# Optimization experiments

Measured on AMD Instinct MI355X. Metric: run time of the kernel, lower is better.

## Reference

```python
import jax, jax.numpy as jnp
import numpy as np

N_HEADS = 16
N_KV_HEADS = 4
WINDOW = 128
THETA = 10000.0


def _rope_cos_sin(T, half):
    inv = 1.0 / (THETA ** (jnp.arange(half, dtype=jnp.float32) / half))
    f = jnp.arange(T, dtype=jnp.float32)[:, None] * inv[None, :]  # (T, half)
    return jnp.cos(f), jnp.sin(f)


def _apply_rope(x, cos, sin):
    # x: (B, H, T, hd); interleaved (real, imag) pairs like torch view_as_complex
    xr, xi = x[..., 0::2], x[..., 1::2]
    out_r = xr * cos - xi * sin
    out_i = xr * sin + xi * cos
    return jnp.stack([out_r, out_i], axis=-1).reshape(x.shape)


def setup_inputs() -> dict:
    key = jax.random.key(0)
    ks = jax.random.split(key, 6)
    B, T, C = 1, 4096, 2048
    kvC = (C // N_HEADS) * N_KV_HEADS
    return {
        "x": jax.random.normal(ks[0], (B, T, C), dtype=jnp.float32),
        "wq": jax.random.normal(ks[1], (C, C), dtype=jnp.float32) * 0.02,
        "wk": jax.random.normal(ks[2], (C, kvC), dtype=jnp.float32) * 0.02,
        "wv": jax.random.normal(ks[3], (C, kvC), dtype=jnp.float32) * 0.02,
        "wo": jax.random.normal(ks[4], (C, C), dtype=jnp.float32) * 0.02,
        "sink": jnp.zeros((1, N_HEADS, 1, 1), dtype=jnp.float32),
    }


def reference(x, wq, wk, wv, wo, sink):
    B, T, C = x.shape
    hd = C // N_HEADS
    n_rep = N_HEADS // N_KV_HEADS

    q = (x @ wq).reshape(B, T, N_HEADS, hd).transpose(0, 2, 1, 3)    # (B,H,T,hd)
    k = (x @ wk).reshape(B, T, N_KV_HEADS, hd).transpose(0, 2, 1, 3)  # (B,Hkv,T,hd)
    v = (x @ wv).reshape(B, T, N_KV_HEADS, hd).transpose(0, 2, 1, 3)

    cos, sin = _rope_cos_sin(T, hd // 2)  # (T, hd/2), broadcasts over (B,H,T,hd/2)
    q = _apply_rope(q, cos, sin)
    k = _apply_rope(k, cos, sin)

    # GQA head expansion (repeat_interleave over head dim)
    k = jnp.repeat(k, n_rep, axis=1)
    v = jnp.repeat(v, n_rep, axis=1)

    att = jnp.einsum("bhqd,bhkd->bhqk", q, k) * (hd ** -0.5) + sink

    # symmetric sliding-window band: |i - j| <= window//2
    idx = jnp.arange(T)
    band = jnp.abs(idx[:, None] - idx[None, :]) <= (WINDOW // 2)
    att = jnp.where(band[None, None, :, :], att, -jnp.inf)

    att = jax.nn.softmax(att, axis=-1)
    # torch code replaces NaN rows (fully-masked) with uniform; band always has diag so no-op
    att = jnp.where(jnp.isnan(att), 1.0 / T, att)

    out = jnp.einsum("bhqk,bhkd->bqhd", att, v).reshape(B, T, C)
    return out @ wo
```

## Files before the change

kernel.cpp:

```cpp
#include <hip/hip_runtime.h>
#include <stdint.h>

#define T_SEQ 4096
#define C_DIM 2048
#define HD 128

typedef unsigned short ushort_t;
typedef __attribute__((ext_vector_type(8))) short shortx8;
typedef __attribute__((ext_vector_type(4))) float floatx4;
typedef __attribute__((ext_vector_type(8))) unsigned short u16x8;
typedef __attribute__((ext_vector_type(4))) unsigned short u16x4;

__device__ __forceinline__ ushort_t f2bf(float f) {
  union { float f; uint32_t u; } v; v.f = f;
  v.u += 0x7fffu + ((v.u >> 16) & 1u);
  return (ushort_t)(v.u >> 16);
}
__device__ __forceinline__ void load_lds16(const ushort_t* g, ushort_t* l) {
  __builtin_amdgcn_global_load_lds(
      (const __attribute__((address_space(1))) unsigned int*)g,
      (__attribute__((address_space(3))) unsigned int*)l, 16, 0, 0);
}

__global__ __launch_bounds__(256) void prep_kernel(
    const float* __restrict__ wq, const float* __restrict__ wk,
    const float* __restrict__ wv, const float* __restrict__ wo,
    const float* __restrict__ x,
    ushort_t* __restrict__ BtAll, ushort_t* __restrict__ woT,
    ushort_t* __restrict__ xb) {
  const int bid = blockIdx.x;
  const int tid = threadIdx.x;
  if (bid >= 2560) {
    int i = (bid - 2560) * 256 + tid;
    float4 v = ((const float4*)x)[i];
    u16x4 o; o[0] = f2bf(v.x); o[1] = f2bf(v.y); o[2] = f2bf(v.z); o[3] = f2bf(v.w);
    ((u16x4*)xb)[i] = o;
    return;
  }
  const float* src; ushort_t* dst; int C, bx, by;
  if (bid < 1024) { src = wq; dst = BtAll; C = 2048; bx = bid & 31; by = bid >> 5; }
  else if (bid < 1280) { int b = bid - 1024; src = wk; dst = BtAll + (size_t)2048 * 2048; C = 512; bx = b & 7; by = b >> 3; }
  else if (bid < 1536) { int b = bid - 1280; src = wv; dst = BtAll + (size_t)2560 * 2048; C = 512; bx = b & 7; by = b >> 3; }
  else { int b = bid - 1536; src = wo; dst = woT; C = 2048; bx = b & 31; by = b >> 5; }
  const int R = 2048;

  __shared__ float tile[64][65];
  const int c0 = bx * 64, r0 = by * 64;
  for (int i = tid; i < 1024; i += 256) {
    int r = i >> 4, cc = (i & 15) * 4;
    float4 v = *(const float4*)&src[(size_t)(r0 + r) * C + c0 + cc];
    tile[r][cc] = v.x; tile[r][cc + 1] = v.y; tile[r][cc + 2] = v.z; tile[r][cc + 3] = v.w;
  }
  __syncthreads();
  for (int i = tid; i < 512; i += 256) {
    int oc = i >> 3;
    int g = (i & 7) * 8;
    u16x8 o;
    for (int j = 0; j < 8; ++j) o[j] = f2bf(tile[g + j][oc]);
    *(u16x8*)&dst[(size_t)(c0 + oc) * R + r0 + g] = o;
  }
}

struct GemmAcc { floatx4 a[4][4]; };

__device__ __forceinline__ void gemm_core_bk64(
    const ushort_t* __restrict__ A, const ushort_t* __restrict__ Bt,
    ushort_t* As, ushort_t* Bs, GemmAcc& acc,
    int m0, int n0, int K, int tid, int lane, int wave, int quad, int l16,
    int wm, int wn) {
  const int nk = K >> 6;
  for (int kk = 0; kk < nk; ++kk) {
    const int k0 = kk << 6;
    for (int r = 0; r < 4; ++r) {
      int e = r * 256 + tid;
      int row = e >> 3;
      int p = e & 7;
      int g = (p - row) & 7;
      const ushort_t* ga = A + (size_t)(m0 + row) * K + k0 + g * 8;
      const ushort_t* gb = Bt + (size_t)(n0 + row) * K + k0 + g * 8;
      ushort_t* la = As + (size_t)(r * 256 + (tid & 192)) * 8;
      ushort_t* lb = Bs + (size_t)(r * 256 + (tid & 192)) * 8;
      load_lds16(ga, la);
      load_lds16(gb, lb);
    }
    __syncthreads();
    for (int ks = 0; ks < 2; ++ks) {
      shortx8 af[4], bfr[4];
      for (int i = 0; i < 4; ++i) {
        int ar = wm + i * 16 + l16;
        af[i] = *(const shortx8*)(As + ar * 64 + (((ks << 2) + quad + ar) & 7) * 8);
        int br = wn + i * 16 + l16;
        bfr[i] = *(const shortx8*)(Bs + br * 64 + (((ks << 2) + quad + br) & 7) * 8);
      }
      for (int i = 0; i < 4; ++i)
        for (int j = 0; j < 4; ++j)
          acc.a[i][j] = __builtin_amdgcn_mfma_f32_16x16x32_bf16(af[i], bfr[j], acc.a[i][j], 0, 0, 0);
    }
    __syncthreads();
  }
}

__global__ __launch_bounds__(256, 3) void gemm_bf16(
    const ushort_t* __restrict__ A, const ushort_t* __restrict__ Bt,
    float* __restrict__ C, int M, int N, int K) {
  __shared__ __align__(16) ushort_t As[128 * 64];
  __shared__ __align__(16) ushort_t Bs[128 * 64];
  const int tid = threadIdx.x;
  const int lane = tid & 63;
  const int wave = tid >> 6;
  const int quad = lane >> 4;
  const int l16 = lane & 15;
  const int m0 = blockIdx.y * 128;
  const int n0 = blockIdx.x * 128;
  const int wm = (wave & 1) * 64;
  const int wn = (wave >> 1) * 64;

  GemmAcc acc = {};
  gemm_core_bk64(A, Bt, As, Bs, acc, m0, n0, K, tid, lane, wave, quad, l16, wm, wn);

  for (int i = 0; i < 4; ++i)
    for (int j = 0; j < 4; ++j) {
      int col = n0 + wn + j * 16 + l16;
      int rbase = m0 + wm + i * 16 + quad * 4;
      for (int r = 0; r < 4; ++r)
        C[(size_t)(rbase + r) * N + col] = acc.a[i][j][r];
    }
}

#define BARF() do { __builtin_amdgcn_s_barrier(); asm volatile("" ::: "memory"); } while (0)

__global__ __launch_bounds__(512, 2) void gemm_qkv256(
    const ushort_t* __restrict__ A, const ushort_t* __restrict__ Bt,
    ushort_t* __restrict__ qbb, ushort_t* __restrict__ kbb,
    ushort_t* __restrict__ vtb) {
  __shared__ __align__(16) ushort_t SA[2][16384];
  __shared__ __align__(16) ushort_t SB[2][16384];
  const int tid = threadIdx.x;
  const int lane = tid & 63;
  const int w = tid >> 6;
  const int l16 = lane & 15;
  const int quad = lane >> 4;
  const int wm = (w >> 2) * 128;
  const int wn = (w & 3) * 64;
  const int aq = wm + (w & 3) * 16;
  const int bq = wn + (w >> 2) * 16;
  const int gl8 = lane >> 3;
  const int gch = ((lane & 7) - gl8) & 7;

  const int bid = blockIdx.x;
  const int swz = (bid & 7) * 24 + (bid >> 3);
  const int n0 = (swz % 12) * 256;
  const int m0 = (swz / 12) * 256;

  const int off0 = l16 * 64 + ((quad + l16) & 7) * 8;
  const int off1 = l16 * 64 + ((4 + quad + l16) & 7) * 8;

  floatx4 acc[8][4] = {};

  auto issue2 = [&](const ushort_t* __restrict__ G, int gRow, ushort_t* L, int r0, int k0) {
#pragma unroll
    for (int u = 0; u < 2; ++u) {
      const ushort_t* src = G + (size_t)(gRow + r0 + u * 8 + gl8) * 2048 + k0 + gch * 8;
      load_lds16(src, L + (r0 + u * 8) * 64);
    }
  };

  issue2(A, m0, SA[0], aq, 0);        issue2(A, m0, SA[0], aq + 64, 0);
  issue2(Bt, n0, SB[0], bq, 0);       issue2(Bt, n0, SB[0], bq + 32, 0);
  issue2(A, m0, SA[1], aq, 64);       issue2(A, m0, SA[1], aq + 64, 64);
  issue2(Bt, n0, SB[1], bq, 64);      issue2(Bt, n0, SB[1], bq + 32, 64);
  asm volatile("s_waitcnt vmcnt(8)" ::: "memory");
  BARF();

  for (int t2 = 0; t2 < 16; ++t2) {
#pragma unroll
    for (int half = 0; half < 2; ++half) {
      const int t = t2 * 2 + half;
      const ushort_t* SAb = SA[half];
      const ushort_t* SBb = SB[half];
      ushort_t* SAo = SA[half ^ 1];
      ushort_t* SBo = SB[half ^ 1];
#pragma unroll
      for (int p = 0; p < 4; ++p) {
        const int ih = p >> 1, jh = p & 1;
        shortx8 af0[4], af1[4], bf0[2], bf1[2];
#pragma unroll
        for (int i2 = 0; i2 < 4; ++i2) {
          const int rb = (wm + (ih * 4 + i2) * 16) * 64;
          af0[i2] = *(const shortx8*)&SAb[rb + off0];
          af1[i2] = *(const shortx8*)&SAb[rb + off1];
        }
#pragma unroll
        for (int j2 = 0; j2 < 2; ++j2) {
          const int rb = (wn + (jh * 2 + j2) * 16) * 64;
          bf0[j2] = *(const shortx8*)&SBb[rb + off0];
          bf1[j2] = *(const shortx8*)&SBb[rb + off1];
        }
        if (p == 0)      { if (t > 0 && t + 1 < 32) issue2(A, m0, SAo, aq + 64, (t + 1) * 64); }
        else if (p == 1) { if (t > 0 && t + 1 < 32) issue2(Bt, n0, SBo, bq + 32, (t + 1) * 64); }
        else if (p == 2) { if (t + 2 < 32) issue2(A, m0, (ushort_t*)SAb, aq, (t + 2) * 64); }
        else             { if (t + 2 < 32) issue2(Bt, n0, (ushort_t*)SBb, bq, (t + 2) * 64); }
        BARF();
        asm volatile("s_waitcnt lgkmcnt(0)" ::: "memory");
        __builtin_amdgcn_s_setprio(1);
#pragma unroll
        for (int ks = 0; ks < 2; ++ks)
#pragma unroll
          for (int i2 = 0; i2 < 4; ++i2)
#pragma unroll
            for (int j2 = 0; j2 < 2; ++j2)
              acc[ih * 4 + i2][jh * 2 + j2] = __builtin_amdgcn_mfma_f32_16x16x32_bf16(
                  ks ? af1[i2] : af0[i2], ks ? bf1[j2] : bf0[j2],
                  acc[ih * 4 + i2][jh * 2 + j2], 0, 0, 0);
        __builtin_amdgcn_s_setprio(0);
        if (p == 3) {
          if (t < 30)       { asm volatile("s_waitcnt vmcnt(4)" ::: "memory"); }
          else if (t == 30) { asm volatile("s_waitcnt vmcnt(0)" ::: "memory"); }
        }
        BARF();
      }
    }
  }

  asm volatile("s_waitcnt vmcnt(0) lgkmcnt(0)" ::: "memory");
  BARF();

  if (n0 < 2560) {
    const bool isq = (n0 < 2048);
    const int par = l16 & 1;
#pragma unroll
    for (int j = 0; j < 4; ++j) {
      int col = n0 + wn + j * 16 + l16;
      int irot = (col & 127) >> 1;
      float inv = __expf(-0.14391157f * (float)irot);
#pragma unroll
      for (int i = 0; i < 8; ++i) {
        int t0r = m0 + wm + i * 16 + quad * 4;
#pragma unroll
        for (int r = 0; r < 4; ++r) {
          float val = acc[i][j][r];
          float other = __shfl_xor(val, 1, 64);
          float sn, cs;
          __sincosf((float)(t0r + r) * inv, &sn, &cs);
          float outv = par ? (other * sn + val * cs) : (val * cs - other * sn);
          if (isq) qbb[(size_t)(t0r + r) * 2048 + col] = f2bf(outv);
          else     kbb[(size_t)(t0r + r) * 512 + (col - 2048)] = f2bf(outv);
        }
      }
    }
  } else {
#pragma unroll
    for (int j = 0; j < 4; ++j) {
      int dim = n0 + wn + j * 16 + l16 - 2560;
#pragma unroll
      for (int i = 0; i < 8; ++i) {
        int t0r = m0 + wm + i * 16 + quad * 4;
        u16x4 o;
#pragma unroll
        for (int r = 0; r < 4; ++r) o[r] = f2bf(acc[i][j][r]);
        *(u16x4*)&vtb[(size_t)dim * T_SEQ + t0r] = o;
      }
    }
  }
}

#define LSTR 168
__global__ __launch_bounds__(256, 2) void attn_kernel(
    const ushort_t* __restrict__ qbb, const ushort_t* __restrict__ kbb,
    const ushort_t* __restrict__ vtb, ushort_t* __restrict__ ao) {
  __shared__ __align__(16) ushort_t QP[64 * LSTR];
  __shared__ __align__(16) ushort_t KV[160 * LSTR];

  const int tid = threadIdx.x;
  const int lane = tid & 63;
  const int wave = tid >> 6;
  const int l16 = lane & 15;
  const int quad = lane >> 4;
  const int h0 = blockIdx.x * 2;
  const int kvh = h0 >> 2;
  const int t0 = blockIdx.y * 32;
  const int kstart = t0 - 64;
  const int hsel = wave & 1;
  const int qh = wave >> 1;
  const float scale = 0.08838834764831845f;

  for (int c = tid; c < 1024; c += 256) {
    int row = c >> 4, c8 = c & 15;
    int h = h0 + (row >> 5);
    int q = t0 + (row & 31);
    u16x8 v = *(const u16x8*)&qbb[(size_t)q * C_DIM + h * HD + c8 * 8];
    *(u16x8*)&QP[row * LSTR + c8 * 8] = v;
  }
  for (int c = tid; c < 2560; c += 256) {
    int row = c >> 4, c8 = c & 15;
    int t = kstart + row;
    u16x8 v;
    if (t >= 0 && t < T_SEQ) {
      v = *(const u16x8*)&kbb[(size_t)t * 512 + kvh * HD + c8 * 8];
    } else {
      for (int z = 0; z < 8; ++z) v[z] = 0;
    }
    *(u16x8*)&KV[row * LSTR + c8 * 8] = v;
  }
  __syncthreads();

  floatx4 acc[10] = {};
  const int arow = hsel * 32 + qh * 16 + l16;
  for (int ks = 0; ks < 4; ++ks) {
    shortx8 af = *(const shortx8*)&QP[arow * LSTR + ks * 32 + quad * 8];
    for (int kt = 0; kt < 10; ++kt) {
      shortx8 bf = *(const shortx8*)&KV[(kt * 16 + l16) * LSTR + ks * 32 + quad * 8];
      acc[kt] = __builtin_amdgcn_mfma_f32_16x16x32_bf16(af, bf, acc[kt], 0, 0, 0);
    }
  }

  float mrow[4] = {-3e38f, -3e38f, -3e38f, -3e38f};
  for (int kt = 0; kt < 10; ++kt) {
    int col = kt * 16 + l16;
    int kg = kstart + col;
    for (int r = 0; r < 4; ++r) {
      int row = qh * 16 + quad * 4 + r;
      bool valid = (kg >= 0) && (kg < T_SEQ) && (col >= row) && (col <= row + 128);
      float s = valid ? acc[kt][r] * scale : -3e38f;
      acc[kt][r] = s;
      mrow[r] = fmaxf(mrow[r], s);
    }
  }
  for (int off = 1; off < 16; off <<= 1)
    for (int r = 0; r < 4; ++r)
      mrow[r] = fmaxf(mrow[r], __shfl_xor(mrow[r], off, 64));
  float rl[4];
  for (int r = 0; r < 4; ++r) {
    float s = 0.f;
    for (int kt = 0; kt < 10; ++kt) {
      float p = __expf(acc[kt][r] - mrow[r]);
      acc[kt][r] = p;
      s += p;
    }
    rl[r] = s;
  }
  for (int off = 1; off < 16; off <<= 1)
    for (int r = 0; r < 4; ++r) rl[r] += __shfl_xor(rl[r], off, 64);
  for (int r = 0; r < 4; ++r) rl[r] = 1.0f / rl[r];

  __syncthreads();

  for (int kt = 0; kt < 10; ++kt) {
    int col = kt * 16 + l16;
    for (int r = 0; r < 4; ++r) {
      int row = hsel * 32 + qh * 16 + quad * 4 + r;
      QP[row * LSTR + col] = f2bf(acc[kt][r] * rl[r]);
    }
  }
  for (int c = tid; c < 2560; c += 256) {
    int dim = c / 20, c8 = c % 20;
    int k0 = kstart + c8 * 8;
    const ushort_t* g = &vtb[(size_t)(kvh * HD + dim) * T_SEQ];
    u16x8 v;
    if (k0 >= 0 && k0 + 7 < T_SEQ) {
      v = *(const u16x8*)&g[k0];
    } else {
      for (int z = 0; z < 8; ++z) {
        int kk = k0 + z;
        v[z] = (kk >= 0 && kk < T_SEQ) ? g[kk] : (ushort_t)0;
      }
    }
    *(u16x8*)&KV[dim * LSTR + c8 * 8] = v;
  }
  __syncthreads();

  floatx4 oacc[8] = {};
  const int prow = hsel * 32 + qh * 16 + l16;
  for (int ks = 0; ks < 5; ++ks) {
    shortx8 pf = *(const shortx8*)&QP[prow * LSTR + ks * 32 + quad * 8];
    for (int dt = 0; dt < 8; ++dt) {
      shortx8 vf = *(const shortx8*)&KV[(dt * 16 + l16) * LSTR + ks * 32 + quad * 8];
      oacc[dt] = __builtin_amdgcn_mfma_f32_16x16x32_bf16(pf, vf, oacc[dt], 0, 0, 0);
    }
  }

  const int h = h0 + hsel;
  for (int r = 0; r < 4; ++r) {
    int row = t0 + qh * 16 + quad * 4 + r;
    for (int dt = 0; dt < 8; ++dt) {
      int dim = dt * 16 + l16;
      ao[(size_t)row * C_DIM + h * HD + dim] = f2bf(oacc[dt][r]);
    }
  }
}

extern "C" void kernel_launch(void* const* d_in, const int* in_sizes, int n_in,
                              void* d_out, int out_size, void* d_ws, size_t ws_size,
                              hipStream_t stream) {
  const float* x  = (const float*)d_in[0];
  const float* wq = (const float*)d_in[1];
  const float* wk = (const float*)d_in[2];
  const float* wv = (const float*)d_in[3];
  const float* wo = (const float*)d_in[4];
  float* out = (float*)d_out;

  char* ws = (char*)d_ws;
  ushort_t* BtAll = (ushort_t*)(ws);
  ushort_t* woT   = (ushort_t*)(ws + 12582912);
  ushort_t* xb    = (ushort_t*)(ws + 20971520);
  ushort_t* qbb   = (ushort_t*)(ws + 37748736);
  ushort_t* kbb   = (ushort_t*)(ws + 54525952);
  ushort_t* vtb   = (ushort_t*)(ws + 58720256);
  ushort_t* ao    = (ushort_t*)(ws + 62914560);

  prep_kernel<<<10752, 256, 0, stream>>>(wq, wk, wv, wo, x, BtAll, woT, xb);

  gemm_qkv256<<<192, 512, 0, stream>>>(xb, BtAll, qbb, kbb, vtb);

  attn_kernel<<<dim3(8, 128), 256, 0, stream>>>(qbb, kbb, vtb, ao);

  gemm_bf16<<<dim3(16, 32), 256, 0, stream>>>(ao, woT, out, 4096, 2048, 2048);
}
```

Baseline: 266.8 us.

## Reorder QKV GEMM sub-tiles to reuse register fragments across phases

```diff
diff --git a/kernel.cpp b/kernel.cpp
--- a/kernel.cpp
+++ b/kernel.cpp
@@ -128,6 +128,7 @@
 }
 
 #define BARF() do { __builtin_amdgcn_s_barrier(); asm volatile("" ::: "memory"); } while (0)
+#define LGKM0() asm volatile("s_waitcnt lgkmcnt(0)" ::: "memory")
 
 __global__ __launch_bounds__(512, 2) void gemm_qkv256(
     const ushort_t* __restrict__ A, const ushort_t* __restrict__ Bt,
@@ -156,6 +157,7 @@
   const int off1 = l16 * 64 + ((4 + quad + l16) & 7) * 8;
 
   floatx4 acc[8][4] = {};
+  shortx8 af0[4], af1[4], bf0[2], bf1[2];
 
   auto issue2 = [&](const ushort_t* __restrict__ G, int gRow, ushort_t* L, int r0, int k0) {
 #pragma unroll
@@ -165,60 +167,74 @@
     }
   };
 
+#define LOAD_A(base, Sb)                                          \
+  _Pragma("unroll")                                               \
+  for (int i2 = 0; i2 < 4; ++i2) {                                \
+    const int rb = (wm + ((base) + i2) * 16) * 64;                \
+    af0[i2] = *(const shortx8*)&(Sb)[rb + off0];                  \
+    af1[i2] = *(const shortx8*)&(Sb)[rb + off1];                  \
+  }
+#define LOAD_B(jb, Sb)                                            \
+  _Pragma("unroll")                                               \
+  for (int j2 = 0; j2 < 2; ++j2) {                                \
+    const int rb = (wn + ((jb) + j2) * 16) * 64;                  \
+    bf0[j2] = *(const shortx8*)&(Sb)[rb + off0];                  \
+    bf1[j2] = *(const shortx8*)&(Sb)[rb + off1];                  \
+  }
+#define MFMA16(ih, jh)                                            \
+  __builtin_amdgcn_s_setprio(1);                                  \
+  _Pragma("unroll")                                               \
+  for (int i2 = 0; i2 < 4; ++i2)                                  \
+    _Pragma("unroll")                                             \
+    for (int j2 = 0; j2 < 2; ++j2) {                              \
+      acc[(ih)*4+i2][(jh)*2+j2] = __builtin_amdgcn_mfma_f32_16x16x32_bf16( \
+          af0[i2], bf0[j2], acc[(ih)*4+i2][(jh)*2+j2], 0, 0, 0);  \
+      acc[(ih)*4+i2][(jh)*2+j2] = __builtin_amdgcn_mfma_f32_16x16x32_bf16( \
+          af1[i2], bf1[j2], acc[(ih)*4+i2][(jh)*2+j2], 0, 0, 0);  \
+    }                                                             \
+  __builtin_amdgcn_s_setprio(0);
+
   issue2(A, m0, SA[0], aq, 0);        issue2(A, m0, SA[0], aq + 64, 0);
   issue2(Bt, n0, SB[0], bq, 0);       issue2(Bt, n0, SB[0], bq + 32, 0);
-  issue2(A, m0, SA[1], aq, 64);       issue2(A, m0, SA[1], aq + 64, 64);
-  issue2(Bt, n0, SB[1], bq, 64);      issue2(Bt, n0, SB[1], bq + 32, 64);
-  asm volatile("s_waitcnt vmcnt(8)" ::: "memory");
+  issue2(A, m0, SA[1], aq + 64, 64);  issue2(Bt, n0, SB[1], bq + 32, 64);
+  asm volatile("s_waitcnt vmcnt(4)" ::: "memory");
   BARF();
 
   for (int t2 = 0; t2 < 16; ++t2) {
 #pragma unroll
     for (int half = 0; half < 2; ++half) {
       const int t = t2 * 2 + half;
-      const ushort_t* SAb = SA[half];
-      const ushort_t* SBb = SB[half];
+      ushort_t* SAb = SA[half];
+      ushort_t* SBb = SB[half];
       ushort_t* SAo = SA[half ^ 1];
       ushort_t* SBo = SB[half ^ 1];
-#pragma unroll
-      for (int p = 0; p < 4; ++p) {
-        const int ih = p >> 1, jh = p & 1;
-        shortx8 af0[4], af1[4], bf0[2], bf1[2];
-#pragma unroll
-        for (int i2 = 0; i2 < 4; ++i2) {
-          const int rb = (wm + (ih * 4 + i2) * 16) * 64;
-          af0[i2] = *(const shortx8*)&SAb[rb + off0];
-          af1[i2] = *(const shortx8*)&SAb[rb + off1];
-        }
-#pragma unroll
-        for (int j2 = 0; j2 < 2; ++j2) {
-          const int rb = (wn + (jh * 2 + j2) * 16) * 64;
-          bf0[j2] = *(const shortx8*)&SBb[rb + off0];
-          bf1[j2] = *(const shortx8*)&SBb[rb + off1];
-        }
-        if (p == 0)      { if (t > 0 && t + 1 < 32) issue2(A, m0, SAo, aq + 64, (t + 1) * 64); }
-        else if (p == 1) { if (t > 0 && t + 1 < 32) issue2(Bt, n0, SBo, bq + 32, (t + 1) * 64); }
-        else if (p == 2) { if (t + 2 < 32) issue2(A, m0, (ushort_t*)SAb, aq, (t + 2) * 64); }
-        else             { if (t + 2 < 32) issue2(Bt, n0, (ushort_t*)SBb, bq, (t + 2) * 64); }
-        BARF();
-        asm volatile("s_waitcnt lgkmcnt(0)" ::: "memory");
-        __builtin_amdgcn_s_setprio(1);
-#pragma unroll
-        for (int ks = 0; ks < 2; ++ks)
-#pragma unroll
-          for (int i2 = 0; i2 < 4; ++i2)
-#pragma unroll
-            for (int j2 = 0; j2 < 2; ++j2)
-              acc[ih * 4 + i2][jh * 2 + j2] = __builtin_amdgcn_mfma_f32_16x16x32_bf16(
-                  ks ? af1[i2] : af0[i2], ks ? bf1[j2] : bf0[j2],
-                  acc[ih * 4 + i2][jh * 2 + j2], 0, 0, 0);
-        __builtin_amdgcn_s_setprio(0);
-        if (p == 3) {
-          if (t < 30)       { asm volatile("s_waitcnt vmcnt(4)" ::: "memory"); }
-          else if (t == 30) { asm volatile("s_waitcnt vmcnt(0)" ::: "memory"); }
-        }
-        BARF();
-      }
+
+      LOAD_A(0, SAb);
+      LOAD_B(0, SBb);
+      if (t + 1 < 32) issue2(A, m0, SAo, aq, (t + 1) * 64);
+      BARF(); LGKM0();
+      MFMA16(0, 0);
+      BARF();
+
+      LOAD_B(2, SBb);
+      if (t + 1 < 32) issue2(Bt, n0, SBo, bq, (t + 1) * 64);
+      BARF(); LGKM0();
+      MFMA16(0, 1);
+      BARF();
+
+      LOAD_A(4, SAb);
+      if (t + 2 < 32) issue2(Bt, n0, SBb, bq + 32, (t + 2) * 64);
+      BARF(); LGKM0();
+      MFMA16(1, 1);
+      BARF();
+
+      LOAD_B(0, SBb);
+      if (t + 2 < 32) issue2(A, m0, SAb, aq + 64, (t + 2) * 64);
+      BARF(); LGKM0();
+      MFMA16(1, 0);
+      if (t < 30)       { asm volatile("s_waitcnt vmcnt(4)" ::: "memory"); }
+      else if (t == 30) { asm volatile("s_waitcnt vmcnt(0)" ::: "memory"); }
+      BARF();
     }
   }
 
@@ -262,6 +278,9 @@
       }
     }
   }
+#undef LOAD_A
+#undef LOAD_B
+#undef MFMA16
 }
 
 #define LSTR 168
```

Result: faster. 258.6 us (-3.1%).
